# Kernel optimization log

Hardware: AMD Instinct MI355X
Metric: run time of the kernel (lower is better)

The kernel has to match this reference:

```python
import jax, jax.numpy as jnp
import numpy as np

NPG = 39      # nodes per graph, from (1+8+64+9)*(39+1)=3280 = lin1 in_features
NEG_SLOPE = 0.2


def gat_conv(x, src, dst, W, a_src, a_dst, b, n):
    """PyG GATConv, heads=1, self-loops already appended to (src, dst).
    x:[N,Fin] W:[Fin,Fout] a_src/a_dst:[Fout] b:[Fout] -> [N,Fout]"""
    h = x @ W                                        # [N,Fout]
    e = jax.nn.leaky_relu(h[src] @ a_src + h[dst] @ a_dst, NEG_SLOPE)  # [E]
    m = jax.lax.stop_gradient(jax.ops.segment_max(e, dst, num_segments=n))
    w = jnp.exp(e - m[dst])
    denom = jax.ops.segment_sum(w, dst, num_segments=n)
    alpha = w / (denom[dst] + 1e-16)                 # segment softmax per target node
    out = jax.ops.segment_sum(alpha[:, None] * h[src], dst, num_segments=n)
    return out + b


def setup_inputs() -> dict:
    key = jax.random.key(0)
    ks = jax.random.split(key, 20)
    B, DEG = 4096, 8
    N = B * NPG
    E = N * DEG
    x = jax.random.normal(ks[0], (N, 1), dtype=jnp.float32)
    # block-diagonal edges: each node emits DEG edges to random nodes in SAME graph
    src = jnp.repeat(jnp.arange(N, dtype=jnp.int64), DEG)
    offs = (src // NPG) * NPG
    dst = offs + jax.random.randint(ks[1], (E,), 0, NPG, dtype=jnp.int64)
    edge_index = jnp.stack([src, dst])
    batch_vec = jnp.repeat(jnp.arange(B, dtype=jnp.int64), NPG)

    def glorot(k, shape):
        fan = shape[0] + (shape[1] if len(shape) > 1 else 1)
        s = jnp.sqrt(6.0 / fan)
        return jax.random.uniform(k, shape, jnp.float32, -s, s)

    p = {
        'W1': glorot(ks[2], (1, 8)),   'a1s': glorot(ks[3], (8,)),  'a1d': glorot(ks[4], (8,)),  'b1': jnp.zeros((8,), jnp.float32),
        'W2': glorot(ks[5], (8, 64)),  'a2s': glorot(ks[6], (64,)), 'a2d': glorot(ks[7], (64,)), 'b2': jnp.zeros((64,), jnp.float32),
        'W3': glorot(ks[8], (64, 9)),  'a3s': glorot(ks[9], (9,)),  'a3d': glorot(ks[10], (9,)), 'b3': jnp.zeros((9,), jnp.float32),
        'lW1': glorot(ks[11], (3280, 5000)), 'lb1': jnp.zeros((5000,), jnp.float32),
        'lW2': glorot(ks[12], (5000, 1024)), 'lb2': jnp.zeros((1024,), jnp.float32),
        'lW3': glorot(ks[13], (1024, 9)),    'lb3': jnp.zeros((9,), jnp.float32),
    }
    return {'x': x, 'edge_index': edge_index, 'batch_vec': batch_vec, **p}


def reference(x, edge_index, batch_vec,
              W1, a1s, a1d, b1, W2, a2s, a2d, b2, W3, a3s, a3d, b3,
              lW1, lb1, lW2, lb2, lW3, lb3):
    N = x.shape[0]
    B = N // NPG
    loops = jnp.arange(N, dtype=edge_index.dtype)
    src = jnp.concatenate([edge_index[0], loops])   # GATConv add_self_loops=True
    dst = jnp.concatenate([edge_index[1], loops])

    res = x.reshape(B, -1)                                    # [B,39]
    out0 = jax.ops.segment_max(x, batch_vec, num_segments=B)  # [B,1]

    h1 = jax.nn.relu(gat_conv(x, src, dst, W1, a1s, a1d, b1, N))   # dropout = eval no-op
    res1 = h1.reshape(B, -1)                                   # [B,312]
    out1 = jax.ops.segment_max(h1, batch_vec, num_segments=B)

    h2 = jax.nn.relu(gat_conv(h1, src, dst, W2, a2s, a2d, b2, N))
    res2 = h2.reshape(B, -1)                                   # [B,2496]
    out2 = jax.ops.segment_max(h2, batch_vec, num_segments=B)

    h3 = jax.nn.relu(gat_conv(h2, src, dst, W3, a3s, a3d, b3, N))
    res3 = h3.reshape(B, -1)                                   # [B,351]
    out3 = jax.ops.segment_max(h3, batch_vec, num_segments=B)

    f = jnp.concatenate([res, res1, res2, res3, out0, out1, out2, out3], axis=1)  # [B,3280]
    f = jax.nn.relu(f @ lW1 + lb1)
    f = jax.nn.relu(f @ lW2 + lb2)
    return f @ lW3 + lb3                                       # [B,9]
```

## Files before the change

kernel.cpp:

```cpp
#include <hip/hip_runtime.h>
#include <hip/hip_bf16.h>
#include <hip/hip_fp16.h>
#include <stdint.h>


typedef float f32x4 __attribute__((ext_vector_type(4)));
typedef short bf16x8 __attribute__((ext_vector_type(8)));
typedef _Float16 f16x8 __attribute__((ext_vector_type(8)));

__device__ __forceinline__ unsigned fenc(float f) {
  int s = __float_as_int(f);
  return s < 0 ? ~(unsigned)s : ((unsigned)s | 0x80000000u);
}
__device__ __forceinline__ float fdec(unsigned u) {
  return (u & 0x80000000u) ? __int_as_float((int)(u & 0x7fffffffu))
                           : __int_as_float(~(int)u);
}


__global__ __launch_bounds__(128) void gnn_block(
    const float* __restrict__ x,
    const int* __restrict__ esrc, const int* __restrict__ edst,
    const float* __restrict__ W1, const float* __restrict__ a1s, const float* __restrict__ a1d, const float* __restrict__ b1,
    const float* __restrict__ W2, const float* __restrict__ a2s, const float* __restrict__ a2d, const float* __restrict__ b2,
    const float* __restrict__ W3, const float* __restrict__ a3s, const float* __restrict__ a3d, const float* __restrict__ b3,
    __hip_bfloat16* __restrict__ fA)
{
  __shared__ __align__(16) float A[1720];
  __shared__ __align__(16) __half Hh2[2816];
  __shared__ __align__(16) __half h1h[320];
  __shared__ __align__(16) float HfT[400];
  __shared__ __align__(16) float sW3T[616];
  __shared__ __align__(16) float xbuf[40];
  __shared__ __align__(16) float a2buf[128];
  __shared__ float sarr[40], darr[40], den[40];
  __shared__ unsigned umax[40];
  __shared__ unsigned umx[132];
  __shared__ float a3sb[12], a3db[12], b3b[12];

  const int tid = threadIdx.x, g = blockIdx.x, w = tid >> 6, f = tid & 63;

  const int rt = g >> 7, mi = (g >> 4) & 7, lrow = g & 15;
  const size_t gbase = (size_t)rt * 52 * 8192 + (size_t)(mi * 2) * 512 + (size_t)lrow * 8;
#define COLADDR(c) (gbase + (size_t)((c) >> 6) * 8192 + (size_t)(((c) >> 5) & 1) * 512 \
                    + (size_t)(((c) >> 3) & 3) * 128 + ((c) & 7))

  for (int i = tid; i < 576; i += 128) { int k = i / 9, f3 = i - 9 * k; sW3T[f3 * 68 + k] = W3[i]; }
  a2buf[tid] = (tid < 64) ? a2s[tid] : a2d[tid - 64];
  if (tid < 9) { a3sb[tid] = a3s[tid]; a3db[tid] = a3d[tid]; b3b[tid] = b3[tid]; }
  for (int i = tid; i < 132; i += 128) umx[i] = 0u;
  for (int i = tid; i < 430; i += 128) *(f32x4*)&A[i * 4] = (f32x4){0.f, 0.f, 0.f, 0.f};
  for (int i = tid; i < 400; i += 128) HfT[i] = 0.f;
  if (tid < 40) { den[tid] = 0.f; umax[tid] = 0u; xbuf[tid] = 0.f; }

  float xv = 0.f;
  if (tid < 39) { xv = x[g * 39 + tid]; xbuf[tid] = xv; fA[COLADDR(tid)] = __float2bfloat16(xv); }

  int els[3], eld[3];
  const int eb = g * 312, nb0 = g * 39;
#pragma unroll
  for (int it = 0; it < 3; ++it) {
    int e = it * 128 + tid, ls = -1, ld = 0;
    if (e < 351) {
      if (e < 312) { ls = esrc[eb + e] - nb0; ld = edst[eb + e] - nb0; }
      else         { ls = e - 312; ld = ls; }
    }
    els[it] = ls; eld[it] = ld;
  }
  float c_s = 0.f, c_d = 0.f;
  const float w1r = W1[tid & 7], b1r = b1[tid & 7];
#pragma unroll
  for (int ff = 0; ff < 8; ++ff) { float wv = W1[ff]; c_s += wv * a1s[ff]; c_d += wv * a1d[ff]; }
  __syncthreads();

  if (tid < 39) atomicMax(&umx[0], fenc(xv));
  float ee[3];
#pragma unroll
  for (int it = 0; it < 3; ++it) {
    if (els[it] >= 0) {
      float e = xbuf[els[it]] * c_s + xbuf[eld[it]] * c_d;
      e = (e > 0.f) ? e : 0.2f * e;
      ee[it] = e;
      atomicMax(&umax[eld[it]], fenc(e));
    }
  }
  __syncthreads();
#pragma unroll
  for (int it = 0; it < 3; ++it) {
    if (els[it] >= 0) {
      float wv = __expf(ee[it] - fdec(umax[eld[it]]));
      atomicAdd(&den[eld[it]], wv);
      atomicAdd(&A[eld[it] * 44 + els[it]], wv);
    }
  }
  __syncthreads();
  if (tid < 39) {
    const float* Ar = &A[tid * 44];
    float q = 0.f;
#pragma unroll
    for (int c = 0; c < 10; ++c) {
      f32x4 a4 = *(const f32x4*)&Ar[c * 4];
      f32x4 x4 = *(const f32x4*)&xbuf[c * 4];
      q += a4.x * x4.x + a4.y * x4.y + a4.z * x4.z + a4.w * x4.w;
    }
    sarr[tid] = q * (1.f / (den[tid] + 1e-16f));
  }
  __syncthreads();
#pragma unroll
  for (int it = 0; it < 3; ++it) {
    int slot = it * 128 + tid;
    if (slot < 312) {
      int i = slot >> 3, fi = slot & 7;
      float v = fmaxf(sarr[i] * w1r + b1r, 0.f);
      h1h[slot] = __float2half(v);
      fA[COLADDR(39 + slot)] = __float2bfloat16(v);
      atomicMax(&umx[1 + fi], fenc(v));
    }
  }
  __syncthreads();

  float ht2r[40];
  {
    float w2k[8];
#pragma unroll
    for (int k = 0; k < 8; ++k) w2k[k] = W2[k * 64 + f];
#pragma unroll
    for (int i = 0; i < 39; ++i) {
      f16x8 hr = *(const f16x8*)&h1h[i * 8];
      float hv = 0.f;
#pragma unroll
      for (int k = 0; k < 8; ++k) hv += (float)hr[k] * w2k[k];
      ht2r[i] = hv;
    }
    ht2r[39] = 0.f;
#pragma unroll
    for (int i = 0; i < 39; ++i) {
      if ((i < 20) ? (w == 0) : (w == 1))
        Hh2[i * 72 + f] = __float2half(ht2r[i]);
    }
    for (int i = tid; i < 430; i += 128) *(f32x4*)&A[i * 4] = (f32x4){0.f, 0.f, 0.f, 0.f};
    if (tid < 39) { den[tid] = 0.f; umax[tid] = 0u; }
  }
  __syncthreads();
  {
    int node = f;
    if (node < 39) {
      const float* ab = a2buf + (tid & 64);
      const __half* hr = &Hh2[node * 72];
      float s = 0.f;
#pragma unroll
      for (int c = 0; c < 8; ++c) {
        f16x8 hv = *(const f16x8*)&hr[c * 8];
        f32x4 a0 = *(const f32x4*)&ab[c * 8];
        f32x4 a1 = *(const f32x4*)&ab[c * 8 + 4];
        s += (float)hv[0] * a0.x + (float)hv[1] * a0.y + (float)hv[2] * a0.z + (float)hv[3] * a0.w
           + (float)hv[4] * a1.x + (float)hv[5] * a1.y + (float)hv[6] * a1.z + (float)hv[7] * a1.w;
      }
      if (tid < 64) sarr[node] = s; else darr[node] = s;
    }
  }
  __syncthreads();
#pragma unroll
  for (int it = 0; it < 3; ++it) {
    if (els[it] >= 0) {
      float e = sarr[els[it]] + darr[eld[it]];
      e = (e > 0.f) ? e : 0.2f * e;
      ee[it] = e;
      atomicMax(&umax[eld[it]], fenc(e));
    }
  }
  __syncthreads();
#pragma unroll
  for (int it = 0; it < 3; ++it) {
    if (els[it] >= 0) {
      float wv = __expf(ee[it] - fdec(umax[eld[it]]));
      atomicAdd(&den[eld[it]], wv);
      atomicAdd(&A[eld[it] * 44 + els[it]], wv);
    }
  }
  __syncthreads();
  {
    const float b2r = b2[f];
    for (int it = 0; it < 20; ++it) {
      int i = it * 2 + w;
      if (i < 39) {
        float inv = 1.f / (den[i] + 1e-16f);
        const float* Ar = &A[i * 44];
        float acc = 0.f;
#pragma unroll
        for (int c = 0; c < 10; ++c) {
          f32x4 a4 = *(const f32x4*)&Ar[c * 4];
          acc += a4.x * ht2r[c * 4] + a4.y * ht2r[c * 4 + 1]
               + a4.z * ht2r[c * 4 + 2] + a4.w * ht2r[c * 4 + 3];
        }
        float v = fmaxf(acc * inv + b2r, 0.f);
        Hh2[i * 72 + f] = __float2half(v);
        fA[COLADDR(351 + i * 64 + f)] = __float2bfloat16(v);
        atomicMax(&umx[9 + f], fenc(v));
      }
    }
  }
  __syncthreads();

  {
#pragma unroll
    for (int it = 0; it < 3; ++it) {
      int slot = it * 128 + tid;
      if (slot < 351) {
        int i = slot / 9, f3 = slot - 9 * i;
        const __half* hr = &Hh2[i * 72];
        const float* wr = &sW3T[f3 * 68];
        float acc = 0.f;
#pragma unroll
        for (int c = 0; c < 8; ++c) {
          f16x8 hv = *(const f16x8*)&hr[c * 8];
          f32x4 w0 = *(const f32x4*)&wr[c * 8];
          f32x4 w1 = *(const f32x4*)&wr[c * 8 + 4];
          acc += (float)hv[0] * w0.x + (float)hv[1] * w0.y + (float)hv[2] * w0.z + (float)hv[3] * w0.w
               + (float)hv[4] * w1.x + (float)hv[5] * w1.y + (float)hv[6] * w1.z + (float)hv[7] * w1.w;
        }
        HfT[f3 * 44 + i] = acc;
      }
    }
    for (int i = tid; i < 430; i += 128) *(f32x4*)&A[i * 4] = (f32x4){0.f, 0.f, 0.f, 0.f};
    if (tid < 39) { den[tid] = 0.f; umax[tid] = 0u; }
  }
  __syncthreads();
  {
    int node = f;
    if (node < 39) {
      const float* av = (tid < 64) ? a3sb : a3db;
      float s = 0.f;
#pragma unroll
      for (int f3 = 0; f3 < 9; ++f3) s += HfT[f3 * 44 + node] * av[f3];
      if (tid < 64) sarr[node] = s; else darr[node] = s;
    }
  }
  __syncthreads();
#pragma unroll
  for (int it = 0; it < 3; ++it) {
    if (els[it] >= 0) {
      float e = sarr[els[it]] + darr[eld[it]];
      e = (e > 0.f) ? e : 0.2f * e;
      ee[it] = e;
      atomicMax(&umax[eld[it]], fenc(e));
    }
  }
  __syncthreads();
#pragma unroll
  for (int it = 0; it < 3; ++it) {
    if (els[it] >= 0) {
      float wv = __expf(ee[it] - fdec(umax[eld[it]]));
      atomicAdd(&den[eld[it]], wv);
      atomicAdd(&A[eld[it] * 44 + els[it]], wv);
    }
  }
  __syncthreads();
#pragma unroll
  for (int it = 0; it < 3; ++it) {
    int slot = it * 128 + tid;
    if (slot < 351) {
      int i = slot / 9, f3 = slot - 9 * i;
      float inv = 1.f / (den[i] + 1e-16f);
      const float* Ar = &A[i * 44];
      const float* Hr = &HfT[f3 * 44];
      float acc = 0.f;
#pragma unroll
      for (int c = 0; c < 10; ++c) {
        f32x4 a4 = *(const f32x4*)&Ar[c * 4];
        f32x4 h4 = *(const f32x4*)&Hr[c * 4];
        acc += a4.x * h4.x + a4.y * h4.y + a4.z * h4.z + a4.w * h4.w;
      }
      float v = fmaxf(acc * inv + b3b[f3], 0.f);
      fA[COLADDR(2847 + slot)] = __float2bfloat16(v);
      atomicMax(&umx[73 + f3], fenc(v));
    }
  }
  __syncthreads();

  if (tid < 130) {
    int c = 3198 + tid;
    float v = (tid < 82) ? fdec(umx[tid]) : 0.f;
    fA[COLADDR(c)] = __float2bfloat16(v);
  }
#undef COLADDR
}


__global__ __launch_bounds__(256) void conv_all(
    const float* __restrict__ lW1, const float* __restrict__ lW2,
    short* __restrict__ W1T, short* __restrict__ W2T)
{
  __shared__ float t[16][260];
  const int bid = blockIdx.x, tid = threadIdx.x;
  const float* W; short* WT; int ktile, ntile, K0, N0, KT;
  if (bid < 4160) { W = lW1; WT = W1T; ktile = bid % 208; ntile = bid / 208; K0 = 3280; N0 = 5000; KT = 52; }
  else { int c2 = bid - 4160; W = lW2; WT = W2T; ktile = c2 % 320; ntile = c2 / 320; K0 = 5000; N0 = 1024; KT = 80; }

  const int kb = ktile * 16, nb = ntile * 256;
  const int wv = tid >> 6, ln = tid & 63;
#pragma unroll
  for (int r = 0; r < 4; ++r) {
    int k = kb + wv * 4 + r;
    int n = nb + ln * 4;
    f32x4 v = (f32x4){0.f, 0.f, 0.f, 0.f};
    if (k < K0 && n < N0) v = *(const f32x4*)&W[(size_t)k * N0 + n];
    *(f32x4*)&t[wv * 4 + r][ln * 4] = v;
  }
  __syncthreads();
#pragma unroll
  for (int h = 0; h < 2; ++h) {
    int c = h * 256 + tid;
    int nl = c >> 1, kc = c & 1;
    int n = nb + nl, k = kb + kc * 8;
    union { bf16x8 v; __hip_bfloat16 b[8]; } z;
#pragma unroll
    for (int j = 0; j < 8; ++j) z.b[j] = __float2bfloat16(t[kc * 8 + j][nl]);
    int rt = n >> 7, mi = (n >> 4) & 7, lr = n & 15;
    int kt = k >> 6, kq = (k >> 5) & 1, lc = (k >> 3) & 3;
    size_t addr = ((((size_t)rt * KT) + kt) * 16 + mi * 2 + kq) * 512 + ((size_t)lr + 16 * lc) * 8;
    *(bf16x8*)&WT[addr] = z.v;
  }
}


__device__ __forceinline__ void gld_lds16(const void* gptr, void* l) {
  typedef const __attribute__((address_space(1))) unsigned int GU;
  typedef __attribute__((address_space(3))) unsigned int LU;
  __builtin_amdgcn_global_load_lds((GU*)gptr, (LU*)l, 16, 0, 0);
}

template<int MODE>
__global__ __launch_bounds__(256) void gemm_tiled(
    const short* __restrict__ A, const short* __restrict__ B,
    const float* __restrict__ bias, int Nreal,
    void* __restrict__ Cout, int Nn, int KT, int ktPerSplit, int outKT)
{
  __shared__ __align__(16) short lA[8192];
  __shared__ __align__(16) short lB[8192];
  const int tid = threadIdx.x;
  const int w = tid >> 6, L = tid & 63;
  const int lrow = L & 15, lch = L >> 4;
  const int mt = blockIdx.y, nt = blockIdx.x;
  const int mw = (w >> 1) * 4, nw = (w & 1) * 4;
  const int kt0 = blockIdx.z * ktPerSplit, kt1 = kt0 + ktPerSplit;

  const short* Ab = A + ((size_t)mt * KT) * 8192 + (size_t)L * 8;
  const short* Bb = B + ((size_t)nt * KT) * 8192 + (size_t)L * 8;

  f32x4 acc[4][4] = {};

  for (int kt = kt0; kt < kt1; ++kt) {
    const short* Ak = Ab + (size_t)kt * 8192;
    const short* Bk = Bb + (size_t)kt * 8192;
#pragma unroll
    for (int j = 0; j < 4; ++j) {
      int st = w * 4 + j;
      gld_lds16(Ak + st * 512, &lA[st * 512]);
      gld_lds16(Bk + st * 512, &lB[st * 512]);
    }
    __syncthreads();
#pragma unroll
    for (int kk = 0; kk < 2; ++kk) {
      bf16x8 af[4], bfr[4];
#pragma unroll
      for (int i = 0; i < 4; ++i) {
        af[i]  = *(const bf16x8*)&lA[((mw + i) * 2 + kk) * 512 + L * 8];
        bfr[i] = *(const bf16x8*)&lB[((nw + i) * 2 + kk) * 512 + L * 8];
      }
#pragma unroll
      for (int i = 0; i < 4; ++i)
#pragma unroll
        for (int j = 0; j < 4; ++j)
          acc[i][j] = __builtin_amdgcn_mfma_f32_16x16x32_bf16(af[i], bfr[j], acc[i][j], 0, 0, 0);
    }
    __syncthreads();
  }

  if (MODE == 0) {
    __hip_bfloat16* C = (__hip_bfloat16*)Cout;
#pragma unroll
    for (int j = 0; j < 4; ++j) {
      int n = nt * 128 + (nw + j) * 16 + lrow;
      float bn = (n < Nreal) ? bias[n] : 0.f;
      int kt = n >> 6, kq = (n >> 5) & 1, lc2 = (n >> 3) & 3, j2 = n & 7;
#pragma unroll
      for (int i = 0; i < 4; ++i) {
        int mi = mw + i;
        size_t base = ((((size_t)mt * outKT + kt) * 16) + mi * 2 + kq) * 512
                      + (size_t)(lch * 4) * 8 + (size_t)lc2 * 128 + j2;
#pragma unroll
        for (int r = 0; r < 4; ++r)
          C[base + r * 8] = __float2bfloat16(fmaxf(acc[i][j][r] + bn, 0.f));
      }
    }
  } else {
    __half* P = (__half*)Cout + (size_t)blockIdx.z * 4096 * 1024;
#pragma unroll
    for (int j = 0; j < 4; ++j) {
      int n = nt * 128 + (nw + j) * 16 + lrow;
#pragma unroll
      for (int i = 0; i < 4; ++i)
#pragma unroll
        for (int r = 0; r < 4; ++r) {
          int m = mt * 128 + (mw + i) * 16 + lch * 4 + r;
          P[(size_t)m * Nn + n] = __float2half(acc[i][j][r]);
        }
    }
  }
}


__global__ __launch_bounds__(256) void gemm3_fused(
    const __half* __restrict__ P,
    const float* __restrict__ b2v,
    const float* __restrict__ W3,
    const float* __restrict__ b3v,
    float* __restrict__ out)
{
  __shared__ float sW3[9 * 1024];
  int tid = threadIdx.x;
  for (int i = tid; i < 9216; i += 256) { int k = i / 9, j = i - 9 * k; sW3[j * 1024 + k] = W3[i]; }
  __syncthreads();
  int row = blockIdx.x * 4 + (tid >> 6);
  int lane = tid & 63;
  const __half* p0 = P + (size_t)row * 1024;
  const size_t S = (size_t)4096 * 1024;
  float acc[9] = {0, 0, 0, 0, 0, 0, 0, 0, 0};
  for (int t = 0; t < 16; ++t) {
    int k = lane + 64 * t;
    float c = __half2float(p0[k]) + __half2float(p0[k + S])
            + __half2float(p0[k + 2 * S]) + __half2float(p0[k + 3 * S]) + b2v[k];
    c = fmaxf(c, 0.f);
#pragma unroll
    for (int j = 0; j < 9; ++j) acc[j] += c * sW3[j * 1024 + k];
  }
#pragma unroll
  for (int j = 0; j < 9; ++j) {
    float v = acc[j];
    v += __shfl_down(v, 32, 64);
    v += __shfl_down(v, 16, 64);
    v += __shfl_down(v, 8, 64);
    v += __shfl_down(v, 4, 64);
    v += __shfl_down(v, 2, 64);
    v += __shfl_down(v, 1, 64);
    if (lane == 0) out[(size_t)row * 9 + j] = v + b3v[j];
  }
}


extern "C" void kernel_launch(void* const* d_in, const int* in_sizes, int n_in,
                              void* d_out, int out_size, void* d_ws, size_t ws_size,
                              hipStream_t stream)
{
  const float* x   = (const float*)d_in[0];
  const int*   ei  = (const int*)d_in[1];
  const float* W1  = (const float*)d_in[3];
  const float* a1s = (const float*)d_in[4];
  const float* a1d = (const float*)d_in[5];
  const float* b1  = (const float*)d_in[6];
  const float* W2  = (const float*)d_in[7];
  const float* a2s = (const float*)d_in[8];
  const float* a2d = (const float*)d_in[9];
  const float* b2  = (const float*)d_in[10];
  const float* W3  = (const float*)d_in[11];
  const float* a3s = (const float*)d_in[12];
  const float* a3d = (const float*)d_in[13];
  const float* b3  = (const float*)d_in[14];
  const float* lW1 = (const float*)d_in[15];
  const float* lb1 = (const float*)d_in[16];
  const float* lW2 = (const float*)d_in[17];
  const float* lb2 = (const float*)d_in[18];
  const float* lW3 = (const float*)d_in[19];
  const float* lb3 = (const float*)d_in[20];

  const int E = 4096 * 39 * 8;
  const int* esrc = ei;
  const int* edst = ei + E;

  short* fA  = (short*)d_ws;
  short* W1T = fA  + (size_t)4096 * 3328;
  short* C1  = W1T + (size_t)5120 * 3328;
  short* W2T = C1  + (size_t)4096 * 5120;
  __half* P  = (__half*)d_ws;

  conv_all<<<5440, 256, 0, stream>>>(lW1, lW2, W1T, W2T);
  gnn_block<<<4096, 128, 0, stream>>>(x, esrc, edst,
                                      W1, a1s, a1d, b1, W2, a2s, a2d, b2, W3, a3s, a3d, b3,
                                      (__hip_bfloat16*)fA);
  gemm_tiled<0><<<dim3(40, 32, 1), 256, 0, stream>>>(fA, W1T, lb1, 5000, C1, 5120, 52, 52, 80);
  gemm_tiled<1><<<dim3(8, 32, 4), 256, 0, stream>>>(C1, W2T, nullptr, 1024, P, 1024, 80, 20, 0);
  gemm3_fused<<<1024, 256, 0, stream>>>(P, lb2, lW3, lb3, (float*)d_out);
}
```

Measured before the change: 491.0 us.

## Fuse weight conversion and GNN blocks into one interleaved launch

Merges the weight transpose/convert kernel and the per-graph GNN kernel into a single launch. Even block ids before 8192 alternate between GNN and conversion work, and the remaining blocks do the leftover conversion tiles. The GNN work is compute/LDS-latency bound while the conversion is memory-bandwidth bound, so co-scheduling them is meant to overlap the two and remove a launch boundary. Conversion blocks now use 128 threads, and all blocks share one LDS union sized for the larger GNN path, which may change occupancy for the conversion part.

After: 536.5 us. 9.3% more time.

```diff
diff --git a/kernel.cpp b/kernel.cpp
--- a/kernel.cpp
+++ b/kernel.cpp
@@ -18,27 +18,75 @@
 }
 
 
-__global__ __launch_bounds__(128) void gnn_block(
+__global__ __launch_bounds__(128) void gnn_conv_fused(
     const float* __restrict__ x,
     const int* __restrict__ esrc, const int* __restrict__ edst,
     const float* __restrict__ W1, const float* __restrict__ a1s, const float* __restrict__ a1d, const float* __restrict__ b1,
     const float* __restrict__ W2, const float* __restrict__ a2s, const float* __restrict__ a2d, const float* __restrict__ b2,
     const float* __restrict__ W3, const float* __restrict__ a3s, const float* __restrict__ a3d, const float* __restrict__ b3,
-    __hip_bfloat16* __restrict__ fA)
+    __hip_bfloat16* __restrict__ fA,
+    const float* __restrict__ lW1, const float* __restrict__ lW2,
+    short* __restrict__ W1T, short* __restrict__ W2T)
 {
-  __shared__ __align__(16) float A[1720];
-  __shared__ __align__(16) __half Hh2[2816];
-  __shared__ __align__(16) __half h1h[320];
-  __shared__ __align__(16) float HfT[400];
-  __shared__ __align__(16) float sW3T[616];
-  __shared__ __align__(16) float xbuf[40];
-  __shared__ __align__(16) float a2buf[128];
-  __shared__ float sarr[40], darr[40], den[40];
-  __shared__ unsigned umax[40];
-  __shared__ unsigned umx[132];
-  __shared__ float a3sb[12], a3db[12], b3b[12];
-
-  const int tid = threadIdx.x, g = blockIdx.x, w = tid >> 6, f = tid & 63;
+  __shared__ __align__(16) char smem[19200];
+  const int tid = threadIdx.x;
+  const int bid = blockIdx.x;
+
+  bool isconv; int idx;
+  if (bid < 8192) { isconv = (bid & 1); idx = bid >> 1; }
+  else { isconv = true; idx = 4096 + (bid - 8192); }
+
+  if (isconv) {
+    float (*t)[260] = (float(*)[260])smem;
+    const int cid = idx;
+    const float* W; short* WT; int ktile, ntile, K0, N0, KT;
+    if (cid < 4160) { W = lW1; WT = W1T; ktile = cid % 208; ntile = cid / 208; K0 = 3280; N0 = 5000; KT = 52; }
+    else { int c2 = cid - 4160; W = lW2; WT = W2T; ktile = c2 % 320; ntile = c2 / 320; K0 = 5000; N0 = 1024; KT = 80; }
+
+    const int kb = ktile * 16, nb = ntile * 256;
+    const int wv = tid >> 6, ln = tid & 63;
+#pragma unroll
+    for (int r = 0; r < 8; ++r) {
+      int k = kb + wv * 8 + r;
+      int n = nb + ln * 4;
+      f32x4 v = (f32x4){0.f, 0.f, 0.f, 0.f};
+      if (k < K0 && n < N0) v = *(const f32x4*)&W[(size_t)k * N0 + n];
+      *(f32x4*)&t[wv * 8 + r][ln * 4] = v;
+    }
+    __syncthreads();
+#pragma unroll
+    for (int h = 0; h < 4; ++h) {
+      int c = h * 128 + tid;
+      int nl = c >> 1, kc = c & 1;
+      int n = nb + nl, k = kb + kc * 8;
+      union { bf16x8 v; __hip_bfloat16 b[8]; } z;
+#pragma unroll
+      for (int j = 0; j < 8; ++j) z.b[j] = __float2bfloat16(t[kc * 8 + j][nl]);
+      int rt = n >> 7, mi = (n >> 4) & 7, lr = n & 15;
+      int kt = k >> 6, kq = (k >> 5) & 1, lc = (k >> 3) & 3;
+      size_t addr = ((((size_t)rt * KT) + kt) * 16 + mi * 2 + kq) * 512 + ((size_t)lr + 16 * lc) * 8;
+      *(bf16x8*)&WT[addr] = z.v;
+    }
+    return;
+  }
+
+  float*    A     = (float*)   (smem);
+  __half*   Hh2   = (__half*)  (smem + 6880);
+  __half*   h1h   = (__half*)  (smem + 12512);
+  float*    HfT   = (float*)   (smem + 13152);
+  float*    sW3T  = (float*)   (smem + 14752);
+  float*    xbuf  = (float*)   (smem + 17216);
+  float*    a2buf = (float*)   (smem + 17376);
+  float*    sarr  = (float*)   (smem + 17888);
+  float*    darr  = (float*)   (smem + 18048);
+  float*    den   = (float*)   (smem + 18208);
+  unsigned* umax  = (unsigned*)(smem + 18368);
+  unsigned* umx   = (unsigned*)(smem + 18528);
+  float*    a3sb  = (float*)   (smem + 19056);
+  float*    a3db  = (float*)   (smem + 19104);
+  float*    b3b   = (float*)   (smem + 19152);
+
+  const int g = idx, w = tid >> 6, f = tid & 63;
 
   const int rt = g >> 7, mi = (g >> 4) & 7, lrow = g & 15;
   const size_t gbase = (size_t)rt * 52 * 8192 + (size_t)(mi * 2) * 512 + (size_t)lrow * 8;
@@ -284,43 +332,6 @@
     fA[COLADDR(c)] = __float2bfloat16(v);
   }
 #undef COLADDR
-}
-
-
-__global__ __launch_bounds__(256) void conv_all(
-    const float* __restrict__ lW1, const float* __restrict__ lW2,
-    short* __restrict__ W1T, short* __restrict__ W2T)
-{
-  __shared__ float t[16][260];
-  const int bid = blockIdx.x, tid = threadIdx.x;
-  const float* W; short* WT; int ktile, ntile, K0, N0, KT;
-  if (bid < 4160) { W = lW1; WT = W1T; ktile = bid % 208; ntile = bid / 208; K0 = 3280; N0 = 5000; KT = 52; }
-  else { int c2 = bid - 4160; W = lW2; WT = W2T; ktile = c2 % 320; ntile = c2 / 320; K0 = 5000; N0 = 1024; KT = 80; }
-
-  const int kb = ktile * 16, nb = ntile * 256;
-  const int wv = tid >> 6, ln = tid & 63;
-#pragma unroll
-  for (int r = 0; r < 4; ++r) {
-    int k = kb + wv * 4 + r;
-    int n = nb + ln * 4;
-    f32x4 v = (f32x4){0.f, 0.f, 0.f, 0.f};
-    if (k < K0 && n < N0) v = *(const f32x4*)&W[(size_t)k * N0 + n];
-    *(f32x4*)&t[wv * 4 + r][ln * 4] = v;
-  }
-  __syncthreads();
-#pragma unroll
-  for (int h = 0; h < 2; ++h) {
-    int c = h * 256 + tid;
-    int nl = c >> 1, kc = c & 1;
-    int n = nb + nl, k = kb + kc * 8;
-    union { bf16x8 v; __hip_bfloat16 b[8]; } z;
-#pragma unroll
-    for (int j = 0; j < 8; ++j) z.b[j] = __float2bfloat16(t[kc * 8 + j][nl]);
-    int rt = n >> 7, mi = (n >> 4) & 7, lr = n & 15;
-    int kt = k >> 6, kq = (k >> 5) & 1, lc = (k >> 3) & 3;
-    size_t addr = ((((size_t)rt * KT) + kt) * 16 + mi * 2 + kq) * 512 + ((size_t)lr + 16 * lc) * 8;
-    *(bf16x8*)&WT[addr] = z.v;
-  }
 }
 
 
@@ -484,10 +495,9 @@
   short* W2T = C1  + (size_t)4096 * 5120;
   __half* P  = (__half*)d_ws;
 
-  conv_all<<<5440, 256, 0, stream>>>(lW1, lW2, W1T, W2T);
-  gnn_block<<<4096, 128, 0, stream>>>(x, esrc, edst,
-                                      W1, a1s, a1d, b1, W2, a2s, a2d, b2, W3, a3s, a3d, b3,
-                                      (__hip_bfloat16*)fA);
+  gnn_conv_fused<<<9536, 128, 0, stream>>>(x, esrc, edst,
+                                           W1, a1s, a1d, b1, W2, a2s, a2d, b2, W3, a3s, a3d, b3,
+                                           (__hip_bfloat16*)fA, lW1, lW2, W1T, W2T);
   gemm_tiled<0><<<dim3(40, 32, 1), 256, 0, stream>>>(fA, W1T, lb1, 5000, C1, 5120, 52, 52, 80);
   gemm_tiled<1><<<dim3(8, 32, 4), 256, 0, stream>>>(C1, W2T, nullptr, 1024, P, 1024, 80, 20, 0);
   gemm3_fused<<<1024, 256, 0, stream>>>(P, lb2, lW3, lb3, (float*)d_out);
```
